# Kernel tuning notes

Measured on AMD Instinct MI355X. Metric: run time of the kernel, lower is better.

The kernel has to match this reference:

```python
import jax, jax.numpy as jnp
import numpy as np

B, S, D = 2, 2048, 1024
H = 16
HD = D // H  # 64
SCALE = HD ** -0.5
EPS = 1e-12  # F.normalize eps


def _rope_sin_cos(length, half, dtype):
    positions = jnp.arange(length, dtype=dtype)
    freqs = jnp.arange(half, dtype=dtype)
    inv_freq = 1.0 / 10000 ** (freqs / max(1, half))
    theta = jnp.einsum('s,f->sf', positions, inv_freq)  # [S, half]
    return jnp.sin(theta)[None, None], jnp.cos(theta)[None, None]  # [1,1,S,half]


def _rotate(x, sin, cos):
    # x: [B,H,S,HD]; interleaved even/odd rotation
    x_even = x[..., 0::2]
    x_odd = x[..., 1::2]
    r_even = x_even * cos - x_odd * sin
    r_odd = x_even * sin + x_odd * cos
    return jnp.stack([r_even, r_odd], axis=-1).reshape(x.shape)


def setup_inputs() -> dict:
    key = jax.random.key(0)
    k1, k2, k3 = jax.random.split(key, 3)
    tokens = jax.random.normal(k1, (B, S, D), dtype=jnp.float32)
    qkv_w = jax.random.normal(k2, (3 * D, D), dtype=jnp.float32) * (D ** -0.5)
    qkv_b = jnp.zeros((3 * D,), dtype=jnp.float32)
    out_w = jax.random.normal(k3, (D, D), dtype=jnp.float32) * (D ** -0.5)
    out_b = jnp.zeros((D,), dtype=jnp.float32)
    return {"tokens": tokens, "qkv_w": qkv_w, "qkv_b": qkv_b,
            "out_w": out_w, "out_b": out_b}


def reference(tokens, qkv_w, qkv_b, out_w, out_b):
    batch, length, _ = tokens.shape
    qkv = tokens @ qkv_w.T + qkv_b                       # [B,S,3D]
    qkv = qkv.reshape(batch, length, 3, H, HD)
    qkv = jnp.transpose(qkv, (0, 3, 1, 2, 4))            # [B,H,S,3,HD]
    q, k, v = qkv[..., 0, :], qkv[..., 1, :], qkv[..., 2, :]
    sin, cos = _rope_sin_cos(length, HD // 2, q.dtype)
    q = _rotate(q, sin, cos)
    k = _rotate(k, sin, cos)
    # QK L2-normalize (F.normalize: x / max(||x||, eps))
    q = q / jnp.maximum(jnp.linalg.norm(q, axis=-1, keepdims=True), EPS)
    k = k / jnp.maximum(jnp.linalg.norm(k, axis=-1, keepdims=True), EPS)
    scores = jnp.einsum('bhqd,bhkd->bhqk', q, k) * SCALE
    attn = jax.nn.softmax(scores, axis=-1)
    out = jnp.einsum('bhqk,bhkd->bhqd', attn, v)          # [B,H,S,HD]
    out = jnp.transpose(out, (0, 2, 1, 3)).reshape(batch, length, D)
    return out @ out_w.T + out_b
```

## Files before the change

### kernel.cpp

```cpp
#include <hip/hip_runtime.h>
#include <hip/hip_bf16.h>
#include <math.h>

#define B_ 2
#define S_ 2048
#define D_ 1024
#define H_ 16
#define HD_ 64
#define BHS (B_*H_*S_)
#define NROWS (B_*S_)

typedef __attribute__((ext_vector_type(8))) short bf16x8;
typedef __attribute__((ext_vector_type(4))) short bf16x4;
typedef __attribute__((ext_vector_type(4))) float f32x4;

#ifdef __HIP_DEVICE_COMPILE__
#if __has_builtin(__builtin_amdgcn_mfma_f32_16x16x16bf16_1k)
#define MFMA16(a, b, c) __builtin_amdgcn_mfma_f32_16x16x16bf16_1k(a, b, c, 0, 0, 0)
#else
#define MFMA16(a, b, c) __builtin_amdgcn_mfma_f32_16x16x16_bf16(a, b, c, 0, 0, 0)
#endif
#define EXP2(x) __builtin_amdgcn_exp2f(x)
#else
#define MFMA16(a, b, c) (c)
#define EXP2(x) exp2f(x)
#endif

#define SCALE_LOG2E 0.18033688011112043f

__device__ __forceinline__ short f2bf(float x) {
  __hip_bfloat16 h = __float2bfloat16(x);
  return *reinterpret_cast<short*>(&h);
}
__device__ __forceinline__ int packbf_hu(float lo, float hi) {
  unsigned lb = __float_as_uint(lo) + 0x8000u;
  unsigned hb = __float_as_uint(hi) + 0x8000u;
  return (int)__builtin_amdgcn_perm(hb, lb, 0x07060302u);
}

__device__ __forceinline__ void gload_lds16(const short* g, short* l) {
  __builtin_amdgcn_global_load_lds(
      (const __attribute__((address_space(1))) void*)g,
      (__attribute__((address_space(3))) void*)l, 16, 0, 0);
}

__global__ __launch_bounds__(256) void prep(
    const float* __restrict__ tokens, const float* __restrict__ qkv_w,
    const float* __restrict__ out_w, short* __restrict__ tok_bf,
    short* __restrict__ qkvw_bf, short* __restrict__ outw_bf,
    float* __restrict__ tab) {
  const int i = blockIdx.x * 256 + threadIdx.x;
  const float* src;
  short* dst;
  int j;
  if (i < 524288) {
    src = tokens; dst = tok_bf; j = i;
  } else if (i < 917504) {
    src = qkv_w; dst = qkvw_bf; j = i - 524288;
  } else if (i < 1048576) {
    src = out_w; dst = outw_bf; j = i - 917504;
  } else if (i < 1056768) {
    const int e = (i - 1048576) * 8;
    const int s = e >> 5;
    const int f0 = e & 31;
#pragma unroll
    for (int k = 0; k < 8; k++) {
      const int f = f0 + k;
      const float theta = (float)s * exp2f(-(float)f * 0.41524101186092034f);
      float sn, cs;
      sincosf(theta, &sn, &cs);
      tab[(s * 32 + f) * 2] = sn;
      tab[(s * 32 + f) * 2 + 1] = cs;
    }
    return;
  } else {
    return;
  }
  const float4 a = *(const float4*)(src + (long)j * 8);
  const float4 b = *(const float4*)(src + (long)j * 8 + 4);
  short tmp[8] = {f2bf(a.x), f2bf(a.y), f2bf(a.z), f2bf(a.w),
                  f2bf(b.x), f2bf(b.y), f2bf(b.z), f2bf(b.w)};
  *(bf16x8*)(dst + (long)j * 8) = *(const bf16x8*)tmp;
}

__global__ __launch_bounds__(256) void qkv_mfma(
    const short* __restrict__ A, const short* __restrict__ W,
    const float* __restrict__ bias, const float* __restrict__ tab,
    short* __restrict__ qb, short* __restrict__ kb, short* __restrict__ vtb) {
  __shared__ short smem[8704];
  short* As = smem;
  short* Bs = smem + 2048;
  const int t = threadIdx.x;
  const int w = t >> 6;
  const int lane = t & 63;
  const int col = lane & 15;
  const int quad = lane >> 4;
  const int wm = w >> 1;
  const int wn = w & 1;
  const int bid = blockIdx.x;
  const int xcd = bid & 7;
  const int seq = bid >> 3;
  const int m0 = (seq / 3) * 64;
  const int n0 = (xcd * 3 + seq % 3) * 128;

  f32x4 acc[2][4] = {};

  for (int k0 = 0; k0 < 1024; k0 += 32) {
    __syncthreads();
    {
      const int c = w * 64 + lane;
      const int row = c >> 2;
      const int gseg = (c & 3) ^ (row & 3);
      gload_lds16(&A[(m0 + row) * 1024 + k0 + gseg * 8], As + w * 512);
    }
#pragma unroll
    for (int i = 0; i < 2; i++) {
      const int c0 = i * 256 + w * 64;
      const int c = c0 + lane;
      const int row = c >> 2;
      const int gseg = (c & 3) ^ (row & 3);
      gload_lds16(&W[(n0 + row) * 1024 + k0 + gseg * 8], Bs + c0 * 8);
    }
    __syncthreads();

    bf16x8 af[2], bfr[4];
#pragma unroll
    for (int mt = 0; mt < 2; mt++) {
      const int m = wm * 32 + mt * 16 + col;
      af[mt] = *(const bf16x8*)&As[m * 32 + ((quad ^ (m & 3)) * 8)];
    }
#pragma unroll
    for (int nt = 0; nt < 4; nt++) {
      const int n = wn * 64 + nt * 16 + col;
      bfr[nt] = *(const bf16x8*)&Bs[n * 32 + ((quad ^ (n & 3)) * 8)];
    }
#pragma unroll
    for (int mt = 0; mt < 2; mt++)
#pragma unroll
      for (int nt = 0; nt < 4; nt++)
        acc[mt][nt] = __builtin_amdgcn_mfma_f32_16x16x32_bf16(
            af[mt], bfr[nt], acc[mt][nt], 0, 0, 0);
  }

  const int j_base = n0 + wn * 64;
  const int c = j_base >> 10;
  const int h = (j_base >> 6) & 15;
  float bi[4];
#pragma unroll
  for (int nt = 0; nt < 4; nt++) bi[nt] = bias[j_base + nt * 16 + col];

  __syncthreads();

  if (c < 2) {
    short* dst = (c == 0) ? qb : kb;
    float* Tf = (float*)smem + w * 1088;
#pragma unroll
    for (int mt = 0; mt < 2; mt++) {
#pragma unroll
      for (int nt = 0; nt < 4; nt++)
#pragma unroll
        for (int r = 0; r < 4; r++)
          Tf[(quad * 4 + r) * 68 + nt * 16 + col] = acc[mt][nt][r] + bi[nt];
#pragma unroll
      for (int p = 0; p < 4; p++) {
        const int rloc = p * 4 + quad;
        const int n = m0 + wm * 32 + mt * 16 + rloc;
        const int bidx = n >> 11;
        const int s = n & 2047;
        const float4 xv = *(const float4*)&Tf[rloc * 68 + col * 4];
        const float4 tc = *(const float4*)&tab[s * 64 + col * 4];
        const float e0 = xv.x * tc.y - xv.y * tc.x;
        const float o0 = xv.x * tc.x + xv.y * tc.y;
        const float e1 = xv.z * tc.w - xv.w * tc.z;
        const float o1 = xv.z * tc.z + xv.w * tc.w;
        float ss = e0 * e0 + o0 * o0 + e1 * e1 + o1 * o1;
        ss += __shfl_xor(ss, 1, 64);
        ss += __shfl_xor(ss, 2, 64);
        ss += __shfl_xor(ss, 4, 64);
        ss += __shfl_xor(ss, 8, 64);
        const float scl = 1.0f / fmaxf(sqrtf(ss), 1e-12f);
        int2 pk;
        pk.x = packbf_hu(e0 * scl, o0 * scl);
        pk.y = packbf_hu(e1 * scl, o1 * scl);
        *(int2*)&dst[((long)(bidx * 16 + h) * 2048 + s) * 64 + col * 4] = pk;
      }
    }
  } else {
    const int bidx = m0 >> 11;
    const int st = (m0 & 2047) >> 6;
    short* vbase = vtb + ((long)(bidx * 16 + h) * 32 + st) * 4096;
#pragma unroll
    for (int mt = 0; mt < 2; mt++)
#pragma unroll
      for (int ntq = 0; ntq < 4; ntq++) {
        int2 pk;
        pk.x = packbf_hu(acc[mt][ntq][0] + bi[ntq], acc[mt][ntq][1] + bi[ntq]);
        pk.y = packbf_hu(acc[mt][ntq][2] + bi[ntq], acc[mt][ntq][3] + bi[ntq]);
        *(int2*)&vbase[(((wm * 2 + mt) * 4 + ntq) * 32 + quad * 8 +
                        (col >> 1)) * 8 + (col & 1) * 4] = pk;
      }
  }
}

__global__ __launch_bounds__(512) void attn_mfma(
    const short* __restrict__ qb,
    const short* __restrict__ kb,
    const short* __restrict__ vt,
    short* __restrict__ ob) {
  __shared__ __align__(16) char smem[35328];
  short* Kf = (short*)smem;
  short* Vf = Kf + 8192;
  const int t = threadIdx.x;
  const int w = t >> 6;
  const int grp = w >> 2;
  const int wl = w & 3;
  const int lane = t & 63;
  const int col = lane & 15;
  const int quad = lane >> 4;
  const int bh = blockIdx.x;
  const int q0 = blockIdx.y * 128;
  const long hb = (long)bh * S_ * 64;
  const short* kg = kb + hb;
  const short* vg = vt + (long)bh * 64 * S_;

  bf16x8 qa[2][2];
#pragma unroll
  for (int mt2 = 0; mt2 < 2; mt2++)
#pragma unroll
    for (int h = 0; h < 2; h++)
      qa[mt2][h] = *(const bf16x8*)&qb[hb +
          (long)(q0 + wl * 32 + mt2 * 16 + col) * 64 + h * 32 + quad * 8];

  const int tt = (wl << 6) | lane;
  int kofs[2];
#pragma unroll
  for (int i = 0; i < 2; i++) {
    const int cc = tt + 256 * i;
    kofs[i] = ((cc >> 7) * 16 + (cc & 15)) * 64 + ((cc >> 6) & 1) * 32 +
              ((cc >> 4) & 3) * 8;
  }

  short* KfL = Kf + grp * 4096;
  short* VfL = Vf + grp * 4096;

  f32x4 oacc[2][4] = {};
  f32x4 lacc[2] = {};
  const short oneb = 0x3F80;
  const bf16x4 ones = {oneb, oneb, oneb, oneb};

  const int kend = grp * 1024 + 1024;
  for (int kt = grp * 1024; kt < kend; kt += 64) {
    __syncthreads();
    const short* kgp = kg + (long)kt * 64;
    const short* vgp = vg + (long)(kt >> 6) * 4096;
#pragma unroll
    for (int i = 0; i < 2; i++) {
      gload_lds16(kgp + kofs[i], KfL + i * 2048 + wl * 512);
      gload_lds16(vgp + (tt + 256 * i) * 8, VfL + i * 2048 + wl * 512);
    }
    __syncthreads();

#pragma unroll
    for (int nt = 0; nt < 4; nt++) {
      const bf16x8 ka0 = *(const bf16x8*)&KfL[nt * 1024 + quad * 128 + col * 8];
      const bf16x8 ka1 =
          *(const bf16x8*)&KfL[nt * 1024 + 512 + quad * 128 + col * 8];
      bf16x4 pb[2];
#pragma unroll
      for (int mt2 = 0; mt2 < 2; mt2++) {
        f32x4 z = {0.f, 0.f, 0.f, 0.f};
        z = __builtin_amdgcn_mfma_f32_16x16x32_bf16(ka0, qa[mt2][0], z, 0, 0, 0);
        z = __builtin_amdgcn_mfma_f32_16x16x32_bf16(ka1, qa[mt2][1], z, 0, 0, 0);
        const float e0 = EXP2(z[0] * SCALE_LOG2E);
        const float e1 = EXP2(z[1] * SCALE_LOG2E);
        const float e2 = EXP2(z[2] * SCALE_LOG2E);
        const float e3 = EXP2(z[3] * SCALE_LOG2E);
        int pk[2] = {packbf_hu(e0, e1), packbf_hu(e2, e3)};
        pb[mt2] = *(const bf16x4*)pk;
        lacc[mt2] = MFMA16(ones, pb[mt2], lacc[mt2]);
      }
#pragma unroll
      for (int dt = 0; dt < 4; dt++) {
        const bf16x4 va =
            *(const bf16x4*)&VfL[(nt * 4 + dt) * 256 + quad * 64 + col * 4];
        oacc[0][dt] = MFMA16(va, pb[0], oacc[0][dt]);
        oacc[1][dt] = MFMA16(va, pb[1], oacc[1][dt]);
      }
    }
  }

  __syncthreads();

  float* Ocomb = (float*)smem;
  float* lsumC = (float*)(smem + 34816);
  if (grp == 1) {
#pragma unroll
    for (int mt2 = 0; mt2 < 2; mt2++) {
      const int qloc = wl * 32 + mt2 * 16 + col;
      if (quad == 0) lsumC[qloc] = lacc[mt2][0];
#pragma unroll
      for (int dt = 0; dt < 4; dt++)
        *(f32x4*)&Ocomb[qloc * 68 + dt * 16 + quad * 4] = oacc[mt2][dt];
    }
  }
  __syncthreads();
  if (grp == 0) {
#pragma unroll
    for (int mt2 = 0; mt2 < 2; mt2++) {
      const int qloc = wl * 32 + mt2 * 16 + col;
      const float inv = 1.0f / (lacc[mt2][0] + lsumC[qloc]);
      short* orow = ob + hb + (long)(q0 + qloc) * 64;
#pragma unroll
      for (int dt = 0; dt < 4; dt++) {
        const float4 oc = *(const float4*)&Ocomb[qloc * 68 + dt * 16 + quad * 4];
        int2 pk;
        pk.x = packbf_hu((oacc[mt2][dt][0] + oc.x) * inv,
                         (oacc[mt2][dt][1] + oc.y) * inv);
        pk.y = packbf_hu((oacc[mt2][dt][2] + oc.z) * inv,
                         (oacc[mt2][dt][3] + oc.w) * inv);
        *(int2*)&orow[dt * 16 + quad * 4] = pk;
      }
    }
  }
}

__global__ __launch_bounds__(256) void out_mfma(
    const short* __restrict__ O, const short* __restrict__ W,
    const float* __restrict__ bias, float* __restrict__ out) {
  __shared__ short As[2048];
  __shared__ short Bs[2048];
  const int t = threadIdx.x;
  const int w = t >> 6;
  const int lane = t & 63;
  const int col = lane & 15;
  const int quad = lane >> 4;
  const int wm = w >> 1;
  const int wn = w & 1;
  const int bid = blockIdx.x;
  const int xcd = bid & 7;
  const int seq = bid >> 3;
  const int m0 = (seq >> 1) * 64;
  const int n0 = (xcd * 2 + (seq & 1)) * 64;

  f32x4 acc[2][2] = {};

  for (int k0 = 0; k0 < 1024; k0 += 32) {
    __syncthreads();
    {
      const int c = w * 64 + lane;
      const int row = c >> 2;
      const int gseg = (c & 3) ^ (row & 3);
      const int n = m0 + row;
      const int bidx = n >> 11;
      const int s = n & 2047;
      const int kk = k0 + gseg * 8;
      gload_lds16(&O[((long)(bidx * 16 + (kk >> 6)) * 2048 + s) * 64 + (kk & 63)],
                  As + w * 512);
    }
    {
      const int c = w * 64 + lane;
      const int row = c >> 2;
      const int gseg = (c & 3) ^ (row & 3);
      gload_lds16(&W[(n0 + row) * 1024 + k0 + gseg * 8], Bs + w * 512);
    }
    __syncthreads();

    bf16x8 af[2], bfr[2];
#pragma unroll
    for (int mt = 0; mt < 2; mt++) {
      const int m = wm * 32 + mt * 16 + col;
      af[mt] = *(const bf16x8*)&As[m * 32 + ((quad ^ (m & 3)) * 8)];
    }
#pragma unroll
    for (int nt = 0; nt < 2; nt++) {
      const int n = wn * 32 + nt * 16 + col;
      bfr[nt] = *(const bf16x8*)&Bs[n * 32 + ((quad ^ (n & 3)) * 8)];
    }
#pragma unroll
    for (int mt = 0; mt < 2; mt++)
#pragma unroll
      for (int nt = 0; nt < 2; nt++)
        acc[mt][nt] = __builtin_amdgcn_mfma_f32_16x16x32_bf16(
            af[mt], bfr[nt], acc[mt][nt], 0, 0, 0);
  }

  float bi[2];
#pragma unroll
  for (int nt = 0; nt < 2; nt++) bi[nt] = bias[n0 + wn * 32 + nt * 16 + col];
#pragma unroll
  for (int mt = 0; mt < 2; mt++) {
#pragma unroll
    for (int r = 0; r < 4; r++) {
      const int n = m0 + wm * 32 + mt * 16 + quad * 4 + r;
#pragma unroll
      for (int nt = 0; nt < 2; nt++)
        out[(long)n * 1024 + n0 + wn * 32 + nt * 16 + col] =
            acc[mt][nt][r] + bi[nt];
    }
  }
}

extern "C" void kernel_launch(void* const* d_in, const int* in_sizes, int n_in,
                              void* d_out, int out_size, void* d_ws,
                              size_t ws_size, hipStream_t stream) {
  const float* tokens = (const float*)d_in[0];
  const float* qkv_w = (const float*)d_in[1];
  const float* qkv_b = (const float*)d_in[2];
  const float* out_w = (const float*)d_in[3];
  const float* out_b = (const float*)d_in[4];
  float* out = (float*)d_out;

  const size_t per = (size_t)BHS * HD_;
  float* tab = (float*)d_ws;
  short* tok_bf = (short*)(tab + 2048 * 64);
  short* qkvw_bf = tok_bf + per;
  short* outw_bf = qkvw_bf + 3 * per / 4;
  short* q_bf = outw_bf + per / 4;
  short* k_bf = q_bf + per;
  short* vt_bf = k_bf + per;
  short* O_bf = vt_bf + per;

  hipLaunchKernelGGL(prep, dim3(4128), dim3(256), 0, stream, tokens, qkv_w,
                     out_w, tok_bf, qkvw_bf, outw_bf, tab);
  hipLaunchKernelGGL(qkv_mfma, dim3(1536), dim3(256), 0, stream, tok_bf,
                     qkvw_bf, qkv_b, tab, q_bf, k_bf, vt_bf);
  hipLaunchKernelGGL(attn_mfma, dim3(B_ * H_, S_ / 128), dim3(512), 0, stream,
                     q_bf, k_bf, vt_bf, O_bf);
  hipLaunchKernelGGL(out_mfma, dim3(1024), dim3(256), 0, stream, O_bf,
                     outw_bf, out_b, out);
}
```

Before: 202.3 us.

## Double-buffer LDS loads in all three kernels and use 16x16x32 MFMA for PV

Adds ping-pong LDS buffers to the QKV GEMM, attention and output GEMM kernels, so the next tile's global-to-LDS load is issued before computing on the current tile. This cuts the number of barriers per tile and hides load latency behind MFMA work. The attention kernel also pairs two key tiles so the PV product and row-sum use the 16x16x32 bf16 MFMA instead of 16x16x16. In exchange, attention LDS grows to 64KB, which may reduce occupancy, and the code carries more register pressure.

```diff
diff --git a/kernel.cpp b/kernel.cpp
--- a/kernel.cpp
+++ b/kernel.cpp
@@ -13,18 +13,15 @@
 typedef __attribute__((ext_vector_type(8))) short bf16x8;
 typedef __attribute__((ext_vector_type(4))) short bf16x4;
 typedef __attribute__((ext_vector_type(4))) float f32x4;
+typedef __attribute__((ext_vector_type(4))) int i32x4;
 
 #ifdef __HIP_DEVICE_COMPILE__
-#if __has_builtin(__builtin_amdgcn_mfma_f32_16x16x16bf16_1k)
-#define MFMA16(a, b, c) __builtin_amdgcn_mfma_f32_16x16x16bf16_1k(a, b, c, 0, 0, 0)
-#else
-#define MFMA16(a, b, c) __builtin_amdgcn_mfma_f32_16x16x16_bf16(a, b, c, 0, 0, 0)
-#endif
 #define EXP2(x) __builtin_amdgcn_exp2f(x)
 #else
-#define MFMA16(a, b, c) (c)
 #define EXP2(x) exp2f(x)
 #endif
+
+#define MFMA32(a, b, c) __builtin_amdgcn_mfma_f32_16x16x32_bf16(a, b, c, 0, 0, 0)
 
 #define SCALE_LOG2E 0.18033688011112043f
 
@@ -87,9 +84,7 @@
     const short* __restrict__ A, const short* __restrict__ W,
     const float* __restrict__ bias, const float* __restrict__ tab,
     short* __restrict__ qb, short* __restrict__ kb, short* __restrict__ vtb) {
-  __shared__ short smem[8704];
-  short* As = smem;
-  short* Bs = smem + 2048;
+  __shared__ short smem[12288];
   const int t = threadIdx.x;
   const int w = t >> 6;
   const int lane = t & 63;
@@ -105,8 +100,7 @@
 
   f32x4 acc[2][4] = {};
 
-  for (int k0 = 0; k0 < 1024; k0 += 32) {
-    __syncthreads();
+  auto stage = [&](short* As, short* Bs, int k0) {
     {
       const int c = w * 64 + lane;
       const int row = c >> 2;
@@ -121,8 +115,9 @@
       const int gseg = (c & 3) ^ (row & 3);
       gload_lds16(&W[(n0 + row) * 1024 + k0 + gseg * 8], Bs + c0 * 8);
     }
-    __syncthreads();
-
+  };
+
+  auto compute = [&](const short* As, const short* Bs) {
     bf16x8 af[2], bfr[4];
 #pragma unroll
     for (int mt = 0; mt < 2; mt++) {
@@ -138,8 +133,24 @@
     for (int mt = 0; mt < 2; mt++)
 #pragma unroll
       for (int nt = 0; nt < 4; nt++)
-        acc[mt][nt] = __builtin_amdgcn_mfma_f32_16x16x32_bf16(
-            af[mt], bfr[nt], acc[mt][nt], 0, 0, 0);
+        acc[mt][nt] = MFMA32(af[mt], bfr[nt], acc[mt][nt]);
+  };
+
+  short* As0 = smem;
+  short* Bs0 = smem + 2048;
+  short* As1 = smem + 6144;
+  short* Bs1 = smem + 8192;
+
+  stage(As0, Bs0, 0);
+  __syncthreads();
+  for (int it = 0; it < 16; it++) {
+    const int k0 = it * 64;
+    stage(As1, Bs1, k0 + 32);
+    compute(As0, Bs0);
+    __syncthreads();
+    if (it < 15) stage(As0, Bs0, k0 + 64);
+    compute(As1, Bs1);
+    __syncthreads();
   }
 
   const int j_base = n0 + wn * 64;
@@ -148,8 +159,6 @@
   float bi[4];
 #pragma unroll
   for (int nt = 0; nt < 4; nt++) bi[nt] = bias[j_base + nt * 16 + col];
-
-  __syncthreads();
 
   if (c < 2) {
     short* dst = (c == 0) ? qb : kb;
@@ -207,9 +216,9 @@
     const short* __restrict__ kb,
     const short* __restrict__ vt,
     short* __restrict__ ob) {
-  __shared__ __align__(16) char smem[35328];
-  short* Kf = (short*)smem;
-  short* Vf = Kf + 8192;
+  __shared__ __align__(16) char smem[65536];
+  short* Ks = (short*)smem;
+  short* Vs = Ks + 16384;
   const int t = threadIdx.x;
   const int w = t >> 6;
   const int grp = w >> 2;
@@ -240,17 +249,17 @@
               ((cc >> 4) & 3) * 8;
   }
 
-  short* KfL = Kf + grp * 4096;
-  short* VfL = Vf + grp * 4096;
+  short* KfL0 = Ks + grp * 4096;
+  short* KfL1 = KfL0 + 8192;
+  short* VfL0 = Vs + grp * 4096;
+  short* VfL1 = VfL0 + 8192;
 
   f32x4 oacc[2][4] = {};
   f32x4 lacc[2] = {};
   const short oneb = 0x3F80;
-  const bf16x4 ones = {oneb, oneb, oneb, oneb};
-
-  const int kend = grp * 1024 + 1024;
-  for (int kt = grp * 1024; kt < kend; kt += 64) {
-    __syncthreads();
+  const bf16x8 ones8 = {oneb, oneb, oneb, oneb, oneb, oneb, oneb, oneb};
+
+  auto stage = [&](short* KfL, short* VfL, int kt) {
     const short* kgp = kg + (long)kt * 64;
     const short* vgp = vg + (long)(kt >> 6) * 4096;
 #pragma unroll
@@ -258,38 +267,66 @@
       gload_lds16(kgp + kofs[i], KfL + i * 2048 + wl * 512);
       gload_lds16(vgp + (tt + 256 * i) * 8, VfL + i * 2048 + wl * 512);
     }
-    __syncthreads();
-
-#pragma unroll
-    for (int nt = 0; nt < 4; nt++) {
-      const bf16x8 ka0 = *(const bf16x8*)&KfL[nt * 1024 + quad * 128 + col * 8];
-      const bf16x8 ka1 =
-          *(const bf16x8*)&KfL[nt * 1024 + 512 + quad * 128 + col * 8];
-      bf16x4 pb[2];
-#pragma unroll
-      for (int mt2 = 0; mt2 < 2; mt2++) {
-        f32x4 z = {0.f, 0.f, 0.f, 0.f};
-        z = __builtin_amdgcn_mfma_f32_16x16x32_bf16(ka0, qa[mt2][0], z, 0, 0, 0);
-        z = __builtin_amdgcn_mfma_f32_16x16x32_bf16(ka1, qa[mt2][1], z, 0, 0, 0);
-        const float e0 = EXP2(z[0] * SCALE_LOG2E);
-        const float e1 = EXP2(z[1] * SCALE_LOG2E);
-        const float e2 = EXP2(z[2] * SCALE_LOG2E);
-        const float e3 = EXP2(z[3] * SCALE_LOG2E);
-        int pk[2] = {packbf_hu(e0, e1), packbf_hu(e2, e3)};
-        pb[mt2] = *(const bf16x4*)pk;
-        lacc[mt2] = MFMA16(ones, pb[mt2], lacc[mt2]);
+  };
+
+  auto compute = [&](const short* KfL, const short* VfL) {
+#pragma unroll
+    for (int ntp = 0; ntp < 2; ntp++) {
+      i32x4 pw[2];
+#pragma unroll
+      for (int half = 0; half < 2; half++) {
+        const int nt = ntp * 2 + half;
+        const bf16x8 ka0 =
+            *(const bf16x8*)&KfL[nt * 1024 + quad * 128 + col * 8];
+        const bf16x8 ka1 =
+            *(const bf16x8*)&KfL[nt * 1024 + 512 + quad * 128 + col * 8];
+#pragma unroll
+        for (int mt2 = 0; mt2 < 2; mt2++) {
+          f32x4 z = {0.f, 0.f, 0.f, 0.f};
+          z = MFMA32(ka0, qa[mt2][0], z);
+          z = MFMA32(ka1, qa[mt2][1], z);
+          const float e0 = EXP2(z[0] * SCALE_LOG2E);
+          const float e1 = EXP2(z[1] * SCALE_LOG2E);
+          const float e2 = EXP2(z[2] * SCALE_LOG2E);
+          const float e3 = EXP2(z[3] * SCALE_LOG2E);
+          if (half == 0) {
+            pw[mt2].x = packbf_hu(e0, e1);
+            pw[mt2].y = packbf_hu(e2, e3);
+          } else {
+            pw[mt2].z = packbf_hu(e0, e1);
+            pw[mt2].w = packbf_hu(e2, e3);
+          }
+        }
       }
+      const bf16x8 pb0 = __builtin_bit_cast(bf16x8, pw[0]);
+      const bf16x8 pb1 = __builtin_bit_cast(bf16x8, pw[1]);
+      lacc[0] = MFMA32(ones8, pb0, lacc[0]);
+      lacc[1] = MFMA32(ones8, pb1, lacc[1]);
 #pragma unroll
       for (int dt = 0; dt < 4; dt++) {
-        const bf16x4 va =
-            *(const bf16x4*)&VfL[(nt * 4 + dt) * 256 + quad * 64 + col * 4];
-        oacc[0][dt] = MFMA16(va, pb[0], oacc[0][dt]);
-        oacc[1][dt] = MFMA16(va, pb[1], oacc[1][dt]);
+        const bf16x4 v0 = *(const bf16x4*)
+            &VfL[((ntp * 2 + 0) * 4 + dt) * 256 + quad * 64 + col * 4];
+        const bf16x4 v1 = *(const bf16x4*)
+            &VfL[((ntp * 2 + 1) * 4 + dt) * 256 + quad * 64 + col * 4];
+        const bf16x8 va = __builtin_shufflevector(v0, v1, 0, 1, 2, 3, 4, 5, 6, 7);
+        oacc[0][dt] = MFMA32(va, pb0, oacc[0][dt]);
+        oacc[1][dt] = MFMA32(va, pb1, oacc[1][dt]);
       }
     }
-  }
-
+  };
+
+  const int base = grp * 1024;
+  stage(KfL0, VfL0, base);
   __syncthreads();
+  for (int it = 0; it < 8; it++) {
+    const int kt0 = base + it * 128;
+    stage(KfL1, VfL1, kt0 + 64);
+    compute(KfL0, VfL0);
+    __syncthreads();
+    if (it < 7) stage(KfL0, VfL0, kt0 + 128);
+    compute(KfL1, VfL1);
+    __syncthreads();
+  }
 
   float* Ocomb = (float*)smem;
   float* lsumC = (float*)(smem + 34816);
@@ -327,8 +364,7 @@
 __global__ __launch_bounds__(256) void out_mfma(
     const short* __restrict__ O, const short* __restrict__ W,
     const float* __restrict__ bias, float* __restrict__ out) {
-  __shared__ short As[2048];
-  __shared__ short Bs[2048];
+  __shared__ short smem[8192];
   const int t = threadIdx.x;
   const int w = t >> 6;
   const int lane = t & 63;
@@ -344,8 +380,7 @@
 
   f32x4 acc[2][2] = {};
 
-  for (int k0 = 0; k0 < 1024; k0 += 32) {
-    __syncthreads();
+  auto stage = [&](short* As, short* Bs, int k0) {
     {
       const int c = w * 64 + lane;
       const int row = c >> 2;
@@ -363,8 +398,9 @@
       const int gseg = (c & 3) ^ (row & 3);
       gload_lds16(&W[(n0 + row) * 1024 + k0 + gseg * 8], Bs + w * 512);
     }
-    __syncthreads();
-
+  };
+
+  auto compute = [&](const short* As, const short* Bs) {
     bf16x8 af[2], bfr[2];
 #pragma unroll
     for (int mt = 0; mt < 2; mt++) {
@@ -380,8 +416,24 @@
     for (int mt = 0; mt < 2; mt++)
 #pragma unroll
       for (int nt = 0; nt < 2; nt++)
-        acc[mt][nt] = __builtin_amdgcn_mfma_f32_16x16x32_bf16(
-            af[mt], bfr[nt], acc[mt][nt], 0, 0, 0);
+        acc[mt][nt] = MFMA32(af[mt], bfr[nt], acc[mt][nt]);
+  };
+
+  short* As0 = smem;
+  short* Bs0 = smem + 2048;
+  short* As1 = smem + 4096;
+  short* Bs1 = smem + 6144;
+
+  stage(As0, Bs0, 0);
+  __syncthreads();
+  for (int it = 0; it < 16; it++) {
+    const int k0 = it * 64;
+    stage(As1, Bs1, k0 + 32);
+    compute(As0, Bs0);
+    __syncthreads();
+    if (it < 15) stage(As0, Bs0, k0 + 64);
+    compute(As1, Bs1);
+    __syncthreads();
   }
 
   float bi[2];
```

Result: faster. 192.3 us (-5.0%).
